# Kernel tuning notes

Hardware: AMD Instinct MI355X
Metric: run time of the kernel (lower is better)

The kernel has to match this reference:

```python
import jax, jax.numpy as jnp
import numpy as np

NUM_NETS = 2_000_000
PINS_PER_NET = 4
NUM_PINS = NUM_NETS * PINS_PER_NET


def setup_inputs() -> dict:
    key = jax.random.key(0)
    k1, k2, k3 = jax.random.split(key, 3)
    num_slrX, num_slrY = 1, 4
    # pin positions already expressed in SLR-grid units: x in [0, num_slrX), y in [0, num_slrY)
    pos = jax.random.uniform(k1, (NUM_PINS, 2), jnp.float32) * jnp.array(
        [float(max(num_slrX, 1)), float(max(num_slrY, 1))], jnp.float32)
    # CSR netpin structure: each net owns PINS_PER_NET pins, flat list is a permutation of all pins
    flat_netpin = jax.random.permutation(k2, NUM_PINS).astype(jnp.int32)
    netpin_start = (jnp.arange(NUM_NETS + 1, dtype=jnp.int32) * PINS_PER_NET)
    net_ids = jnp.repeat(jnp.arange(NUM_NETS, dtype=jnp.int32), PINS_PER_NET)
    net_weights = jax.random.uniform(k3, (NUM_NETS,), jnp.float32, minval=0.5, maxval=1.5)
    net_mask = jnp.ones((NUM_NETS,), jnp.bool_)
    pin_mask = jnp.zeros((NUM_PINS,), jnp.bool_)
    inv_gamma = jnp.float32(2.0)  # 1 / gamma, gamma = 0.5
    return dict(pos=pos, flat_netpin=flat_netpin, netpin_start=netpin_start,
                net_ids=net_ids, net_weights=net_weights, net_mask=net_mask,
                pin_mask=pin_mask, inv_gamma=inv_gamma,
                num_slrX=num_slrX, num_slrY=num_slrY)


def reference(pos, flat_netpin, netpin_start, net_ids, net_weights, net_mask,
              pin_mask, inv_gamma, num_slrX, num_slrY):
    """Weighted-average SLL: per-net log-sum-exp weighted-average span of pin
    SLR coordinates, per dimension, counted only for dims with >1 SLR."""
    n = net_weights.shape[0]
    p = pos[flat_netpin]  # [P, 2] gather pin coords in CSR order
    # numerically-stable exp weights per net (segment max/min shift)
    mx = jax.ops.segment_max(p, net_ids, num_segments=n)  # [N, 2]
    mn = jax.ops.segment_min(p, net_ids, num_segments=n)  # [N, 2]
    ep = jnp.exp((p - mx[net_ids]) * inv_gamma)   # exp(+x/gamma), shifted
    en = jnp.exp((mn[net_ids] - p) * inv_gamma)   # exp(-x/gamma), shifted
    s_ep = jax.ops.segment_sum(ep, net_ids, num_segments=n)
    s_xep = jax.ops.segment_sum(p * ep, net_ids, num_segments=n)
    s_en = jax.ops.segment_sum(en, net_ids, num_segments=n)
    s_xen = jax.ops.segment_sum(p * en, net_ids, num_segments=n)
    wa = s_xep / s_ep - s_xen / s_en  # [N, 2] weighted-average span per dim
    dim_on = jnp.array([num_slrX > 1, num_slrY > 1], dtype=wa.dtype)  # only multi-SLR dims
    per_net = jnp.sum(wa * dim_on, axis=1)  # [N]
    return jnp.sum(jnp.where(net_mask, net_weights * per_net, jnp.float32(0.0)))
```

## Files before the change

### kernel.cpp

```cpp
#include <hip/hip_runtime.h>
#include <stdint.h>


#define PINB_SHIFT 13
#define PINB_SIZE  (1 << PINB_SHIFT)
#define MAX_PINB   1024
#define JB_SHIFT   14
#define JB_SIZE    (1 << JB_SHIFT)
#define MAX_JB     512
#define P1_CHUNK   8192
#define P2_CHUNK   4096

__device__ __forceinline__ float wa4(float a, float b, float c, float d, float ig) {
    float ea = __expf(a * ig), eb = __expf(b * ig);
    float ec = __expf(c * ig), ed = __expf(d * ig);
    float na = __expf(-a * ig), nb = __expf(-b * ig);
    float nc = __expf(-c * ig), nd = __expf(-d * ig);
    float s_ep  = ea + eb + ec + ed;
    float s_xep = a * ea + b * eb + c * ec + d * ed;
    float s_en  = na + nb + nc + nd;
    float s_xen = a * na + b * nb + c * nc + d * nd;
    return s_xep / s_ep - s_xen / s_en;
}

__global__ void init_kernel(unsigned* __restrict__ cur1, int n_pinb,
                            unsigned* __restrict__ cur2, int n_jb,
                            float* __restrict__ out) {
    int t = threadIdx.x;
    if (t == 0) out[0] = 0.0f;
    for (int i = t; i < n_pinb; i += blockDim.x) cur1[i] = (unsigned)i << PINB_SHIFT;
    for (int i = t; i < n_jb;   i += blockDim.x) cur2[i] = (unsigned)i << JB_SHIFT;
}

__global__ void reinit_cur2_kernel(unsigned* __restrict__ cur2, int n_jb) {
    int t = threadIdx.x;
    for (int i = t; i < n_jb; i += blockDim.x) cur2[i] = (unsigned)i << JB_SHIFT;
}

__global__ __launch_bounds__(512) void p1_partition(
    const int4* __restrict__ fnp4, int NP, int n_pinb,
    uint2* __restrict__ ent1, unsigned* __restrict__ cur1)
{
    __shared__ uint2    staged[P1_CHUNK];
    __shared__ unsigned hist[MAX_PINB];
    __shared__ unsigned scn[MAX_PINB];
    __shared__ unsigned gbase[MAX_PINB];
    const int base  = blockIdx.x * P1_CHUNK;
    const int valid = min(P1_CHUNK, NP - base);
    const int t = threadIdx.x;

    for (int b = t; b < MAX_PINB; b += 512) hist[b] = 0;
    __syncthreads();

    unsigned pin[16], rnk[16];
    #pragma unroll
    for (int m4 = 0; m4 < 4; ++m4) {
        int k4 = t + 512 * m4;
        int kk = 4 * k4;
        int4 v = make_int4(0, 0, 0, 0);
        if (kk < valid) v = fnp4[(base >> 2) + k4];
        pin[4*m4+0] = (unsigned)v.x; pin[4*m4+1] = (unsigned)v.y;
        pin[4*m4+2] = (unsigned)v.z; pin[4*m4+3] = (unsigned)v.w;
    }
    #pragma unroll
    for (int m4 = 0; m4 < 4; ++m4)
        #pragma unroll
        for (int c = 0; c < 4; ++c) {
            int kk = 4 * (t + 512 * m4) + c;
            rnk[4*m4+c] = 0;
            if (kk < valid)
                rnk[4*m4+c] = atomicAdd(&hist[pin[4*m4+c] >> PINB_SHIFT], 1u);
        }
    __syncthreads();

    if (t < 64) {
        unsigned v[16], s = 0;
        #pragma unroll
        for (int i = 0; i < 16; ++i) { v[i] = hist[t * 16 + i]; s += v[i]; }
        unsigned e = s;
        #pragma unroll
        for (int off = 1; off < 64; off <<= 1) {
            unsigned u = __shfl_up(e, off, 64);
            if (t >= off) e += u;
        }
        e -= s;
        #pragma unroll
        for (int i = 0; i < 16; ++i) { scn[t * 16 + i] = e; e += v[i]; }
    }
    __syncthreads();
    for (int b = t; b < n_pinb; b += 512)
        if (hist[b]) gbase[b] = atomicAdd(&cur1[b], hist[b]);
    __syncthreads();

    #pragma unroll
    for (int m4 = 0; m4 < 4; ++m4)
        #pragma unroll
        for (int c = 0; c < 4; ++c) {
            int kk = 4 * (t + 512 * m4) + c;
            if (kk < valid) {
                unsigned p = pin[4*m4+c];
                staged[scn[p >> PINB_SHIFT] + rnk[4*m4+c]] =
                    make_uint2(p, (unsigned)(base + kk));
            }
        }
    __syncthreads();

    for (int k = t; k < valid; k += 512) {
        uint2 e = staged[k];
        unsigned b = e.x >> PINB_SHIFT;
        ent1[gbase[b] + ((unsigned)k - scn[b])] = e;
    }
}

__global__ __launch_bounds__(512) void p2_gather(
    const uint2* __restrict__ ent1, const float2* __restrict__ pos2,
    const int* __restrict__ slrx_p, const int* __restrict__ slry_p,
    int d, int NP, int n_jb,
    uint2* __restrict__ ent2, unsigned* __restrict__ cur2)
{
    const int slr = (d == 0) ? slrx_p[0] : slry_p[0];
    if (slr <= 1) return;

    __shared__ float    win[PINB_SIZE];
    __shared__ uint2    staged[P2_CHUNK];
    __shared__ unsigned hist[MAX_JB], scn[MAX_JB], gbase[MAX_JB];
    const int b       = blockIdx.x;
    const int pbase   = b << PINB_SHIFT;
    const int count_b = min(PINB_SIZE, NP - pbase);
    const int t = threadIdx.x;

    for (int i = t; i < count_b; i += 512) {
        float2 p = pos2[pbase + i];
        win[i] = d ? p.y : p.x;
    }

    #pragma unroll
    for (int r = 0; r < PINB_SIZE / P2_CHUNK; ++r) {
        const int cbase = r * P2_CHUNK;
        const int valid = min(P2_CHUNK, count_b - cbase);
        __syncthreads();
        for (int q = t; q < MAX_JB; q += 512) hist[q] = 0;
        __syncthreads();

        uint2 e[8]; unsigned rnk[8]; float yv[8];
        #pragma unroll
        for (int m = 0; m < 8; ++m) {
            int k = t + 512 * m;
            e[m] = make_uint2(0u, 0u);
            if (k < valid) e[m] = ent1[pbase + cbase + k];
        }
        #pragma unroll
        for (int m = 0; m < 8; ++m) {
            int k = t + 512 * m;
            yv[m] = (k < valid) ? win[e[m].x - (unsigned)pbase] : 0.0f;
        }
        #pragma unroll
        for (int m = 0; m < 8; ++m) {
            int k = t + 512 * m;
            rnk[m] = 0;
            if (k < valid) rnk[m] = atomicAdd(&hist[e[m].y >> JB_SHIFT], 1u);
        }
        __syncthreads();

        if (t < 64) {
            unsigned v[8], s = 0;
            #pragma unroll
            for (int i = 0; i < 8; ++i) { v[i] = hist[t * 8 + i]; s += v[i]; }
            unsigned ex = s;
            #pragma unroll
            for (int off = 1; off < 64; off <<= 1) {
                unsigned u = __shfl_up(ex, off, 64);
                if (t >= off) ex += u;
            }
            ex -= s;
            #pragma unroll
            for (int i = 0; i < 8; ++i) { scn[t * 8 + i] = ex; ex += v[i]; }
        }
        __syncthreads();
        if (t < n_jb && hist[t]) gbase[t] = atomicAdd(&cur2[t], hist[t]);
        __syncthreads();

        #pragma unroll
        for (int m = 0; m < 8; ++m) {
            int k = t + 512 * m;
            if (k < valid)
                staged[scn[e[m].y >> JB_SHIFT] + rnk[m]] =
                    make_uint2(e[m].y, __float_as_uint(yv[m]));
        }
        __syncthreads();

        for (int k = t; k < valid; k += 512) {
            uint2 s2 = staged[k];
            unsigned jb = s2.x >> JB_SHIFT;
            ent2[gbase[jb] + ((unsigned)k - scn[jb])] = s2;
        }
    }
}

__global__ __launch_bounds__(512) void p3_compute(
    const uint2* __restrict__ ent2, const float* __restrict__ wts,
    const float* __restrict__ ig_p,
    const int* __restrict__ slrx_p, const int* __restrict__ slry_p,
    int d, int NP, float* __restrict__ out)
{
    const int slr = (d == 0) ? slrx_p[0] : slry_p[0];
    if (slr <= 1) return;

    __shared__ float ytmp[JB_SIZE];
    const int jb     = blockIdx.x;
    const int base_j = jb << JB_SHIFT;
    const int nslots = min(JB_SIZE, NP - base_j);
    const int t = threadIdx.x;
    const float ig = ig_p[0];

    for (int k = t; k < nslots; k += 512) {
        uint2 e = ent2[base_j + k];
        ytmp[e.x & (JB_SIZE - 1)] = __uint_as_float(e.y);
    }
    __syncthreads();

    float val = 0.0f;
    const int nnets = nslots >> 2, bnet = base_j >> 2;
    const float4* y4 = (const float4*)ytmp;
    for (int i = t; i < nnets; i += 512) {
        float4 p = y4[i];
        val += wts[bnet + i] * wa4(p.x, p.y, p.z, p.w, ig);
    }

    #pragma unroll
    for (int off = 32; off > 0; off >>= 1) val += __shfl_down(val, off, 64);
    __syncthreads();
    if ((t & 63) == 0) ytmp[t >> 6] = val;
    __syncthreads();
    if (t == 0) {
        float s = 0.0f;
        #pragma unroll
        for (int w = 0; w < 8; ++w) s += ytmp[w];
        atomicAdd(out, s);
    }
}

__global__ __launch_bounds__(256) void wasll_fallback(
    const float2* __restrict__ pos, const int4* __restrict__ fnp4,
    const float* __restrict__ net_weights, const float* __restrict__ inv_gamma_p,
    const int* __restrict__ slrx_p, const int* __restrict__ slry_p,
    float* __restrict__ out, int num_nets)
{
    const float ig = inv_gamma_p[0];
    const float dx = (slrx_p[0] > 1) ? 1.0f : 0.0f;
    const float dy = (slry_p[0] > 1) ? 1.0f : 0.0f;
    int net = blockIdx.x * blockDim.x + threadIdx.x;
    float val = 0.0f;
    if (net < num_nets) {
        int4 idx = fnp4[net];
        float2 p0 = pos[idx.x], p1 = pos[idx.y], p2 = pos[idx.z], p3 = pos[idx.w];
        val = net_weights[net] * (dx * wa4(p0.x, p1.x, p2.x, p3.x, ig)
                                + dy * wa4(p0.y, p1.y, p2.y, p3.y, ig));
    }
    #pragma unroll
    for (int off = 32; off > 0; off >>= 1) val += __shfl_down(val, off, 64);
    __shared__ float smem[4];
    if ((threadIdx.x & 63) == 0) smem[threadIdx.x >> 6] = val;
    __syncthreads();
    if (threadIdx.x == 0)
        atomicAdd(out, smem[0] + smem[1] + smem[2] + smem[3]);
}

__global__ void zero_out_kernel(float* __restrict__ out) { out[0] = 0.0f; }

extern "C" void kernel_launch(void* const* d_in, const int* in_sizes, int n_in,
                              void* d_out, int out_size, void* d_ws, size_t ws_size,
                              hipStream_t stream) {
    const float* posf        = (const float*)d_in[0];
    const int*   fnp         = (const int*)d_in[1];
    const float* net_weights = (const float*)d_in[4];
    const float* inv_gamma   = (const float*)d_in[7];
    const int*   slrx        = (const int*)d_in[8];
    const int*   slry        = (const int*)d_in[9];
    float*       out         = (float*)d_out;
    const int    N  = in_sizes[4];
    const int    NP = in_sizes[1];

    const int n_pinb = (NP + PINB_SIZE - 1) >> PINB_SHIFT;
    const int n_jb   = (NP + JB_SIZE - 1) >> JB_SHIFT;

    size_t off = 0;
    auto carve = [&](size_t bytes) { size_t o = off; off += (bytes + 255) & ~size_t(255); return o; };
    size_t o_ent1 = carve((size_t)n_pinb * PINB_SIZE * sizeof(uint2));
    size_t o_ent2 = carve((size_t)n_jb * JB_SIZE * sizeof(uint2));
    size_t o_cur1 = carve((size_t)n_pinb * sizeof(unsigned));
    size_t o_cur2 = carve((size_t)n_jb * sizeof(unsigned));

    const bool ok = (NP == 4 * N) && (NP % 4 == 0) &&
                    (n_pinb <= MAX_PINB) && (n_jb <= MAX_JB) && (off <= ws_size);
    if (!ok) {
        hipLaunchKernelGGL(zero_out_kernel, dim3(1), dim3(1), 0, stream, out);
        const int block = 256, grid = (N + block - 1) / block;
        hipLaunchKernelGGL(wasll_fallback, dim3(grid), dim3(block), 0, stream,
                           (const float2*)posf, (const int4*)fnp, net_weights,
                           inv_gamma, slrx, slry, out, N);
        return;
    }

    char* ws = (char*)d_ws;
    uint2*    ent1 = (uint2*)(ws + o_ent1);
    uint2*    ent2 = (uint2*)(ws + o_ent2);
    unsigned* cur1 = (unsigned*)(ws + o_cur1);
    unsigned* cur2 = (unsigned*)(ws + o_cur2);

    hipLaunchKernelGGL(init_kernel, dim3(1), dim3(1024), 0, stream,
                       cur1, n_pinb, cur2, n_jb, out);

    const int g1 = (NP + P1_CHUNK - 1) / P1_CHUNK;
    hipLaunchKernelGGL(p1_partition, dim3(g1), dim3(512), 0, stream,
                       (const int4*)fnp, NP, n_pinb, ent1, cur1);

    hipLaunchKernelGGL(p2_gather, dim3(n_pinb), dim3(512), 0, stream,
                       ent1, (const float2*)posf, slrx, slry, 0, NP, n_jb, ent2, cur2);
    hipLaunchKernelGGL(p3_compute, dim3(n_jb), dim3(512), 0, stream,
                       ent2, net_weights, inv_gamma, slrx, slry, 0, NP, out);

    hipLaunchKernelGGL(reinit_cur2_kernel, dim3(1), dim3(1024), 0, stream, cur2, n_jb);

    hipLaunchKernelGGL(p2_gather, dim3(n_pinb), dim3(512), 0, stream,
                       ent1, (const float2*)posf, slrx, slry, 1, NP, n_jb, ent2, cur2);
    hipLaunchKernelGGL(p3_compute, dim3(n_jb), dim3(512), 0, stream,
                       ent2, net_weights, inv_gamma, slrx, slry, 1, NP, out);
}
```

Baseline: 278.2 us.

## Use 1024-thread blocks, fold global atomics into scan, drop cur2 reinit kernel

Raises block size from 512 to 1024 threads in all three pipeline kernels, so each thread holds fewer entries in registers. The per-bucket global atomicAdd for reserving output slots now runs inside the 64-thread scan loop, with a precomputed offset stored in hist. This removes the gbase array and one barrier. A second cur2 cursor array is initialised up front, which eliminates the separate reinit kernel launch between dimensions. The cost is that the global atomics are serialized across only 64 threads, and larger blocks may hurt scheduling or spill.

Result: slower. 724.1 us (+160.2%).

```diff
diff --git a/kernel.cpp b/kernel.cpp
--- a/kernel.cpp
+++ b/kernel.cpp
@@ -10,6 +10,7 @@
 #define MAX_JB     512
 #define P1_CHUNK   8192
 #define P2_CHUNK   4096
+#define NTHR       1024
 
 __device__ __forceinline__ float wa4(float a, float b, float c, float d, float ig) {
     float ea = __expf(a * ig), eb = __expf(b * ig);
@@ -29,33 +30,30 @@
     int t = threadIdx.x;
     if (t == 0) out[0] = 0.0f;
     for (int i = t; i < n_pinb; i += blockDim.x) cur1[i] = (unsigned)i << PINB_SHIFT;
-    for (int i = t; i < n_jb;   i += blockDim.x) cur2[i] = (unsigned)i << JB_SHIFT;
-}
-
-__global__ void reinit_cur2_kernel(unsigned* __restrict__ cur2, int n_jb) {
-    int t = threadIdx.x;
-    for (int i = t; i < n_jb; i += blockDim.x) cur2[i] = (unsigned)i << JB_SHIFT;
-}
-
-__global__ __launch_bounds__(512) void p1_partition(
+    for (int i = t; i < 2 * n_jb; i += blockDim.x) {
+        int j = (i < n_jb) ? i : (i - n_jb);
+        cur2[i] = (unsigned)j << JB_SHIFT;
+    }
+}
+
+__global__ __launch_bounds__(NTHR, 8) void p1_partition(
     const int4* __restrict__ fnp4, int NP, int n_pinb,
     uint2* __restrict__ ent1, unsigned* __restrict__ cur1)
 {
     __shared__ uint2    staged[P1_CHUNK];
     __shared__ unsigned hist[MAX_PINB];
     __shared__ unsigned scn[MAX_PINB];
-    __shared__ unsigned gbase[MAX_PINB];
     const int base  = blockIdx.x * P1_CHUNK;
     const int valid = min(P1_CHUNK, NP - base);
     const int t = threadIdx.x;
 
-    for (int b = t; b < MAX_PINB; b += 512) hist[b] = 0;
-    __syncthreads();
-
-    unsigned pin[16], rnk[16];
-    #pragma unroll
-    for (int m4 = 0; m4 < 4; ++m4) {
-        int k4 = t + 512 * m4;
+    if (t < MAX_PINB) hist[t] = 0;
+    __syncthreads();
+
+    unsigned pin[8], rnk[8];
+    #pragma unroll
+    for (int m4 = 0; m4 < 2; ++m4) {
+        int k4 = t + NTHR * m4;
         int kk = 4 * k4;
         int4 v = make_int4(0, 0, 0, 0);
         if (kk < valid) v = fnp4[(base >> 2) + k4];
@@ -63,10 +61,10 @@
         pin[4*m4+2] = (unsigned)v.z; pin[4*m4+3] = (unsigned)v.w;
     }
     #pragma unroll
-    for (int m4 = 0; m4 < 4; ++m4)
+    for (int m4 = 0; m4 < 2; ++m4)
         #pragma unroll
         for (int c = 0; c < 4; ++c) {
-            int kk = 4 * (t + 512 * m4) + c;
+            int kk = 4 * (t + NTHR * m4) + c;
             rnk[4*m4+c] = 0;
             if (kk < valid)
                 rnk[4*m4+c] = atomicAdd(&hist[pin[4*m4+c] >> PINB_SHIFT], 1u);
@@ -85,18 +83,20 @@
         }
         e -= s;
         #pragma unroll
-        for (int i = 0; i < 16; ++i) { scn[t * 16 + i] = e; e += v[i]; }
-    }
-    __syncthreads();
-    for (int b = t; b < n_pinb; b += 512)
-        if (hist[b]) gbase[b] = atomicAdd(&cur1[b], hist[b]);
-    __syncthreads();
-
-    #pragma unroll
-    for (int m4 = 0; m4 < 4; ++m4)
+        for (int i = 0; i < 16; ++i) {
+            scn[t * 16 + i] = e;
+            unsigned g = v[i] ? atomicAdd(&cur1[t * 16 + i], v[i]) : 0u;
+            hist[t * 16 + i] = g - e;
+            e += v[i];
+        }
+    }
+    __syncthreads();
+
+    #pragma unroll
+    for (int m4 = 0; m4 < 2; ++m4)
         #pragma unroll
         for (int c = 0; c < 4; ++c) {
-            int kk = 4 * (t + 512 * m4) + c;
+            int kk = 4 * (t + NTHR * m4) + c;
             if (kk < valid) {
                 unsigned p = pin[4*m4+c];
                 staged[scn[p >> PINB_SHIFT] + rnk[4*m4+c]] =
@@ -105,14 +105,14 @@
         }
     __syncthreads();
 
-    for (int k = t; k < valid; k += 512) {
+    for (int k = t; k < valid; k += NTHR) {
         uint2 e = staged[k];
         unsigned b = e.x >> PINB_SHIFT;
-        ent1[gbase[b] + ((unsigned)k - scn[b])] = e;
-    }
-}
-
-__global__ __launch_bounds__(512) void p2_gather(
+        ent1[hist[b] + (unsigned)k] = e;
+    }
+}
+
+__global__ __launch_bounds__(NTHR, 8) void p2_gather(
     const uint2* __restrict__ ent1, const float2* __restrict__ pos2,
     const int* __restrict__ slrx_p, const int* __restrict__ slry_p,
     int d, int NP, int n_jb,
@@ -123,13 +123,13 @@
 
     __shared__ float    win[PINB_SIZE];
     __shared__ uint2    staged[P2_CHUNK];
-    __shared__ unsigned hist[MAX_JB], scn[MAX_JB], gbase[MAX_JB];
+    __shared__ unsigned hist[MAX_JB], scn[MAX_JB];
     const int b       = blockIdx.x;
     const int pbase   = b << PINB_SHIFT;
     const int count_b = min(PINB_SIZE, NP - pbase);
     const int t = threadIdx.x;
 
-    for (int i = t; i < count_b; i += 512) {
+    for (int i = t; i < count_b; i += NTHR) {
         float2 p = pos2[pbase + i];
         win[i] = d ? p.y : p.x;
     }
@@ -139,24 +139,24 @@
         const int cbase = r * P2_CHUNK;
         const int valid = min(P2_CHUNK, count_b - cbase);
         __syncthreads();
-        for (int q = t; q < MAX_JB; q += 512) hist[q] = 0;
-        __syncthreads();
-
-        uint2 e[8]; unsigned rnk[8]; float yv[8];
-        #pragma unroll
-        for (int m = 0; m < 8; ++m) {
-            int k = t + 512 * m;
+        if (t < MAX_JB) hist[t] = 0;
+        __syncthreads();
+
+        uint2 e[4]; unsigned rnk[4]; float yv[4];
+        #pragma unroll
+        for (int m = 0; m < 4; ++m) {
+            int k = t + NTHR * m;
             e[m] = make_uint2(0u, 0u);
             if (k < valid) e[m] = ent1[pbase + cbase + k];
         }
         #pragma unroll
-        for (int m = 0; m < 8; ++m) {
-            int k = t + 512 * m;
+        for (int m = 0; m < 4; ++m) {
+            int k = t + NTHR * m;
             yv[m] = (k < valid) ? win[e[m].x - (unsigned)pbase] : 0.0f;
         }
         #pragma unroll
-        for (int m = 0; m < 8; ++m) {
-            int k = t + 512 * m;
+        for (int m = 0; m < 4; ++m) {
+            int k = t + NTHR * m;
             rnk[m] = 0;
             if (k < valid) rnk[m] = atomicAdd(&hist[e[m].y >> JB_SHIFT], 1u);
         }
@@ -174,30 +174,33 @@
             }
             ex -= s;
             #pragma unroll
-            for (int i = 0; i < 8; ++i) { scn[t * 8 + i] = ex; ex += v[i]; }
-        }
-        __syncthreads();
-        if (t < n_jb && hist[t]) gbase[t] = atomicAdd(&cur2[t], hist[t]);
-        __syncthreads();
-
-        #pragma unroll
-        for (int m = 0; m < 8; ++m) {
-            int k = t + 512 * m;
+            for (int i = 0; i < 8; ++i) {
+                scn[t * 8 + i] = ex;
+                unsigned g = v[i] ? atomicAdd(&cur2[t * 8 + i], v[i]) : 0u;
+                hist[t * 8 + i] = g - ex;
+                ex += v[i];
+            }
+        }
+        __syncthreads();
+
+        #pragma unroll
+        for (int m = 0; m < 4; ++m) {
+            int k = t + NTHR * m;
             if (k < valid)
                 staged[scn[e[m].y >> JB_SHIFT] + rnk[m]] =
                     make_uint2(e[m].y, __float_as_uint(yv[m]));
         }
         __syncthreads();
 
-        for (int k = t; k < valid; k += 512) {
+        for (int k = t; k < valid; k += NTHR) {
             uint2 s2 = staged[k];
             unsigned jb = s2.x >> JB_SHIFT;
-            ent2[gbase[jb] + ((unsigned)k - scn[jb])] = s2;
-        }
-    }
-}
-
-__global__ __launch_bounds__(512) void p3_compute(
+            ent2[hist[jb] + (unsigned)k] = s2;
+        }
+    }
+}
+
+__global__ __launch_bounds__(NTHR, 8) void p3_compute(
     const uint2* __restrict__ ent2, const float* __restrict__ wts,
     const float* __restrict__ ig_p,
     const int* __restrict__ slrx_p, const int* __restrict__ slry_p,
@@ -213,7 +216,7 @@
     const int t = threadIdx.x;
     const float ig = ig_p[0];
 
-    for (int k = t; k < nslots; k += 512) {
+    for (int k = t; k < nslots; k += NTHR) {
         uint2 e = ent2[base_j + k];
         ytmp[e.x & (JB_SIZE - 1)] = __uint_as_float(e.y);
     }
@@ -222,7 +225,7 @@
     float val = 0.0f;
     const int nnets = nslots >> 2, bnet = base_j >> 2;
     const float4* y4 = (const float4*)ytmp;
-    for (int i = t; i < nnets; i += 512) {
+    for (int i = t; i < nnets; i += NTHR) {
         float4 p = y4[i];
         val += wts[bnet + i] * wa4(p.x, p.y, p.z, p.w, ig);
     }
@@ -235,7 +238,7 @@
     if (t == 0) {
         float s = 0.0f;
         #pragma unroll
-        for (int w = 0; w < 8; ++w) s += ytmp[w];
+        for (int w = 0; w < 16; ++w) s += ytmp[w];
         atomicAdd(out, s);
     }
 }
@@ -289,7 +292,7 @@
     size_t o_ent1 = carve((size_t)n_pinb * PINB_SIZE * sizeof(uint2));
     size_t o_ent2 = carve((size_t)n_jb * JB_SIZE * sizeof(uint2));
     size_t o_cur1 = carve((size_t)n_pinb * sizeof(unsigned));
-    size_t o_cur2 = carve((size_t)n_jb * sizeof(unsigned));
+    size_t o_cur2 = carve((size_t)2 * n_jb * sizeof(unsigned));
 
     const bool ok = (NP == 4 * N) && (NP % 4 == 0) &&
                     (n_pinb <= MAX_PINB) && (n_jb <= MAX_JB) && (off <= ws_size);
@@ -312,18 +315,16 @@
                        cur1, n_pinb, cur2, n_jb, out);
 
     const int g1 = (NP + P1_CHUNK - 1) / P1_CHUNK;
-    hipLaunchKernelGGL(p1_partition, dim3(g1), dim3(512), 0, stream,
+    hipLaunchKernelGGL(p1_partition, dim3(g1), dim3(NTHR), 0, stream,
                        (const int4*)fnp, NP, n_pinb, ent1, cur1);
 
-    hipLaunchKernelGGL(p2_gather, dim3(n_pinb), dim3(512), 0, stream,
+    hipLaunchKernelGGL(p2_gather, dim3(n_pinb), dim3(NTHR), 0, stream,
                        ent1, (const float2*)posf, slrx, slry, 0, NP, n_jb, ent2, cur2);
-    hipLaunchKernelGGL(p3_compute, dim3(n_jb), dim3(512), 0, stream,
+    hipLaunchKernelGGL(p3_compute, dim3(n_jb), dim3(NTHR), 0, stream,
                        ent2, net_weights, inv_gamma, slrx, slry, 0, NP, out);
 
-    hipLaunchKernelGGL(reinit_cur2_kernel, dim3(1), dim3(1024), 0, stream, cur2, n_jb);
-
-    hipLaunchKernelGGL(p2_gather, dim3(n_pinb), dim3(512), 0, stream,
-                       ent1, (const float2*)posf, slrx, slry, 1, NP, n_jb, ent2, cur2);
-    hipLaunchKernelGGL(p3_compute, dim3(n_jb), dim3(512), 0, stream,
+    hipLaunchKernelGGL(p2_gather, dim3(n_pinb), dim3(NTHR), 0, stream,
+                       ent1, (const float2*)posf, slrx, slry, 1, NP, n_jb, ent2, cur2 + n_jb);
+    hipLaunchKernelGGL(p3_compute, dim3(n_jb), dim3(NTHR), 0, stream,
                        ent2, net_weights, inv_gamma, slrx, slry, 1, NP, out);
 }
```
